# Kernel tuning notes

Measured on AMD Instinct MI355X. Metric: run time of the kernel, lower is better.

The kernel has to match this reference:

```python
import jax, jax.numpy as jnp
import numpy as np

EPS = 1e-6


def setup_inputs() -> dict:
    key = jax.random.key(0)
    ks = jax.random.split(key, 7)
    T, B, D, N = 512, 32, 1024, 128
    scale_w = (6.0 / (N + D)) ** 0.5  # xavier_uniform bound
    def w(k):
        return jax.random.uniform(k, (N, D), jnp.float32, -scale_w, scale_w)
    return {
        "x": jax.random.normal(ks[0], (T, B, D), jnp.float32),
        "S0": jnp.zeros((B, N, N), jnp.float32),
        "W_k": w(ks[1]),
        "W_v": w(ks[2]),
        "W_q": w(ks[3]),
        "W_erase": w(ks[4]),
        "W_write": w(ks[5]),
    }


def _ntm_forward(x, S0, W_k, W_v, W_q, W_erase, W_write):
    # Projections for all timesteps at once: (T, B, n_state)
    k = jnp.einsum('tbd,nd->tbn', x, W_k)
    v = jnp.einsum('tbd,nd->tbn', x, W_v)
    q = jnp.einsum('tbd,nd->tbn', x, W_q)
    erase = jnp.einsum('tbd,nd->tbn', x, W_erase)  # use_sigmoid=False: raw
    write = jnp.einsum('tbd,nd->tbn', x, W_write)

    def step(S, inp):
        k_t, v_t, q_t, e_t, w_t = inp
        k_norm = k_t / (jnp.linalg.norm(k_t, axis=-1, keepdims=True) + EPS)
        # S: (B, n, n); outer products via broadcasting
        erase_outer = e_t[:, :, None] * k_norm[:, None, :]
        write_outer = (w_t * v_t)[:, :, None] * k_norm[:, None, :]
        S_new = jnp.tanh(S * (1.0 - erase_outer) + write_outer)
        Sq = jnp.einsum('bij,bj->bi', S_new, q_t)
        out = Sq * jax.nn.silu(Sq)
        return S_new, out

    S_final, outputs = jax.lax.scan(step, S0, (k, v, q, erase, write))
    return outputs, S_final


def reference(x, S0, W_k, W_v, W_q, W_erase, W_write):
    return _ntm_forward(x, S0, W_k, W_v, W_q, W_erase, W_write)
```

## Files before the change

### kernel.cpp

```cpp
#include <hip/hip_runtime.h>
#include <hip/hip_bf16.h>


typedef __attribute__((ext_vector_type(8))) short bf16x8;
typedef __attribute__((ext_vector_type(4))) float f32x4;
typedef __attribute__((ext_vector_type(2))) float f32x2;
typedef __attribute__((ext_vector_type(4))) unsigned short u16x4;

static constexpr int T_STEPS = 512;
static constexpr int BATCH   = 32;
static constexpr int DDIM    = 1024;
static constexpr int NDIM    = 128;
static constexpr int LDC     = 5 * NDIM;
static constexpr int MROWS   = T_STEPS * BATCH;
static constexpr int OUT_N   = T_STEPS * BATCH * NDIM;

__device__ __forceinline__ void split2(float v, unsigned short& hi, unsigned short& lo) {
    unsigned u  = __builtin_bit_cast(unsigned, v);
    unsigned uh = u & 0xFFFF0000u;
    hi = (unsigned short)(uh >> 16);
    float d = v - __builtin_bit_cast(float, uh);
    lo = (unsigned short)(__builtin_bit_cast(unsigned, d) >> 16);
}

static constexpr int LSTR = 40;
static constexpr int OAH = 0, OAL = 128 * LSTR, OBH = 2 * 128 * LSTR, OBL = 3 * 128 * LSTR;

__global__ __launch_bounds__(256, 3) void gemm_kernel(
    const float* __restrict__ x,
    const float* __restrict__ w0, const float* __restrict__ w1,
    const float* __restrict__ w2, const float* __restrict__ w3,
    const float* __restrict__ w4,
    float* __restrict__ C)
{
    __shared__ unsigned short lds[4 * 128 * LSTR];

    const float* Ws[5] = {w0, w1, w2, w3, w4};
    const int id  = blockIdx.x;
    const int xcd = id & 7;
    const int kq  = id >> 3;
    const int bn  = kq % 5;
    const int bm  = (kq / 5) * 8 + xcd;

    const int tid  = threadIdx.x;
    const int wave = tid >> 6, lane = tid & 63;
    const int quad = lane >> 4, l16 = lane & 15;
    const int wm = (wave >> 1) * 64, wn = (wave & 1) * 64;
    const int m0 = bm * 128;
    const float* wsrc = Ws[bn];

    f32x4 acc[4][4];
#pragma unroll
    for (int i = 0; i < 4; ++i)
#pragma unroll
        for (int j = 0; j < 4; ++j) acc[i][j] = (f32x4)(0.0f);

    const int srow = tid >> 3;
    const int sc4  = tid & 7;
    const int fa = (wm + l16) * LSTR + quad * 8;
    const int fb = (wn + l16) * LSTR + quad * 8;

    for (int kk = 0; kk < 32; ++kk) {
#pragma unroll
        for (int i = 0; i < 4; ++i) {
            const int row = srow + i * 32;
            f32x4 va = *(const f32x4*)(x + (size_t)(m0 + row) * DDIM + kk * 32 + sc4 * 4);
            f32x4 vb = *(const f32x4*)(wsrc + (size_t)row * DDIM + kk * 32 + sc4 * 4);
            u16x4 ha, la, hb, lb;
#pragma unroll
            for (int j = 0; j < 4; ++j) {
                unsigned short h, l;
                split2(va[j], h, l); ha[j] = h; la[j] = l;
                split2(vb[j], h, l); hb[j] = h; lb[j] = l;
            }
            const int o = row * LSTR + sc4 * 4;
            *(u16x4*)&lds[OAH + o] = ha;
            *(u16x4*)&lds[OAL + o] = la;
            *(u16x4*)&lds[OBH + o] = hb;
            *(u16x4*)&lds[OBL + o] = lb;
        }
        __syncthreads();

        bf16x8 ah[4], al[4], bh[4], bl[4];
#pragma unroll
        for (int i = 0; i < 4; ++i) {
            ah[i] = *(const bf16x8*)&lds[OAH + fa + i * 16 * LSTR];
            al[i] = *(const bf16x8*)&lds[OAL + fa + i * 16 * LSTR];
            bh[i] = *(const bf16x8*)&lds[OBH + fb + i * 16 * LSTR];
            bl[i] = *(const bf16x8*)&lds[OBL + fb + i * 16 * LSTR];
        }
#pragma unroll
        for (int mi = 0; mi < 4; ++mi)
#pragma unroll
            for (int ni = 0; ni < 4; ++ni) {
                acc[mi][ni] = __builtin_amdgcn_mfma_f32_16x16x32_bf16(
                    ah[mi], bh[ni], acc[mi][ni], 0, 0, 0);
                acc[mi][ni] = __builtin_amdgcn_mfma_f32_16x16x32_bf16(
                    ah[mi], bl[ni], acc[mi][ni], 0, 0, 0);
                acc[mi][ni] = __builtin_amdgcn_mfma_f32_16x16x32_bf16(
                    al[mi], bh[ni], acc[mi][ni], 0, 0, 0);
            }
        __syncthreads();
    }

#pragma unroll
    for (int mi = 0; mi < 4; ++mi)
#pragma unroll
        for (int ni = 0; ni < 4; ++ni) {
            const int row = m0 + wm + mi * 16 + quad * 4;
            const int col = bn * 128 + wn + ni * 16 + l16;
#pragma unroll
            for (int r = 0; r < 4; ++r)
                C[(size_t)(row + r) * LDC + col] = acc[mi][ni][r];
        }
}

__global__ __launch_bounds__(256) void knorm_kernel(float* __restrict__ C)
{
    const int r    = blockIdx.x * 4 + (threadIdx.x >> 6);
    const int lane = threadIdx.x & 63;
    float* base = C + (size_t)r * LDC;

    f32x2 k2 = *(const f32x2*)(base + lane * 2);
    f32x2 v2 = *(const f32x2*)(base + NDIM + lane * 2);
    f32x2 w2 = *(const f32x2*)(base + 4 * NDIM + lane * 2);

    float ss = k2.x * k2.x + k2.y * k2.y;
#pragma unroll
    for (int off = 32; off >= 1; off >>= 1) ss += __shfl_xor(ss, off, 64);
    float inv = __builtin_amdgcn_rcpf(sqrtf(ss) + 1e-6f);

    f32x2 kn = {k2.x * inv, k2.y * inv};
    f32x2 wv = {v2.x * w2.x, v2.y * w2.y};
    *(f32x2*)(base + lane * 2) = kn;
    *(f32x2*)(base + NDIM + lane * 2) = wv;
}

__device__ __forceinline__ float tanh_fast(float xx) {
    float ex = __builtin_amdgcn_exp2f(xx * 2.8853900817779268f);
    float r  = __builtin_amdgcn_rcpf(ex + 1.0f);
    return fmaf(-2.0f, r, 1.0f);
}

template <int CTRL, int RMASK>
__device__ __forceinline__ float dpp_add(float x) {
    int yi = __builtin_amdgcn_update_dpp(
        0, __builtin_bit_cast(int, x), CTRL, RMASK, 0xF, true);
    return x + __builtin_bit_cast(float, yi);
}

__device__ __forceinline__ float dpp_reduce32(float x) {
    x = dpp_add<0xB1,  0xF>(x);
    x = dpp_add<0x4E,  0xF>(x);
    x = dpp_add<0x141, 0xF>(x);
    x = dpp_add<0x140, 0xF>(x);
    x = dpp_add<0x142, 0xA>(x);
    return x;
}

__global__ __launch_bounds__(256) void ntm_scan_kernel(
    const float* __restrict__ C, const float* __restrict__ S0,
    float* __restrict__ out)
{
    const int L    = blockIdx.x;
    const int b    = (L & 7) + 8 * ((L >> 3) & 3);
    const int row  = (L >> 5) * 8 + (threadIdx.x >> 5);
    const int g    = threadIdx.x & 31;
    const int col0 = g * 4;

    f32x4 S = *(const f32x4*)(S0 + ((size_t)b * NDIM + row) * NDIM + col0);

    const size_t STRIDE = (size_t)BATCH * LDC;
    const float* pb = C + (size_t)b * LDC;

    f32x4 kS[4], qS[4];
    float eS[4], wvS[4];

#pragma unroll
    for (int s = 0; s < 2; ++s) {
        const float* p = pb + (size_t)s * STRIDE;
        kS[s]  = *(const f32x4*)(p + col0);
        qS[s]  = *(const f32x4*)(p + 2 * NDIM + col0);
        eS[s]  = p[3 * NDIM + row];
        wvS[s] = p[NDIM + row];
    }

    float* op = out + (size_t)b * NDIM + row;

    for (int ti = 0; ti < T_STEPS / 4; ++ti) {
#pragma unroll
        for (int j = 0; j < 4; ++j) {
            const int t = ti * 4 + j;
            {
                int tp = t + 2;
                if (tp > T_STEPS - 1) tp = T_STEPS - 1;
                const float* p = pb + (size_t)tp * STRIDE;
                const int ps = (j + 2) & 3;
                kS[ps]  = *(const f32x4*)(p + col0);
                qS[ps]  = *(const f32x4*)(p + 2 * NDIM + col0);
                eS[ps]  = p[3 * NDIM + row];
                wvS[ps] = p[NDIM + row];
            }
            float dot = 0.0f;
#pragma unroll
            for (int u = 0; u < 4; ++u) {
                float t0  = fmaf(-eS[j], S[u], wvS[j]);
                float pre = fmaf(kS[j][u], t0, S[u]);
                S[u] = tanh_fast(pre);
                dot = fmaf(S[u], qS[j][u], dot);
            }
            dot = dpp_reduce32(dot);

            if ((threadIdx.x & 31) == 31)
                op[(size_t)t * BATCH * NDIM] = dot;
        }
    }

    *(f32x4*)(out + (size_t)T_STEPS * BATCH * NDIM
              + ((size_t)b * NDIM + row) * NDIM + col0) = S;
}

__global__ __launch_bounds__(256) void silu_kernel(float* __restrict__ out)
{
    const int i = blockIdx.x * 256 + threadIdx.x;
    f32x4 d = ((const f32x4*)out)[i];
    f32x4 y;
#pragma unroll
    for (int j = 0; j < 4; ++j) {
        float sg = __builtin_amdgcn_rcpf(
            1.0f + __builtin_amdgcn_exp2f(-d[j] * 1.4426950408889634f));
        y[j] = d[j] * d[j] * sg;
    }
    ((f32x4*)out)[i] = y;
}

extern "C" void kernel_launch(void* const* d_in, const int* in_sizes, int n_in,
                              void* d_out, int out_size, void* d_ws, size_t ws_size,
                              hipStream_t stream) {
    const float* x  = (const float*)d_in[0];
    const float* S0 = (const float*)d_in[1];
    const float* wk = (const float*)d_in[2];
    const float* wv = (const float*)d_in[3];
    const float* wq = (const float*)d_in[4];
    const float* we = (const float*)d_in[5];
    const float* ww = (const float*)d_in[6];
    float* out = (float*)d_out;
    float* C   = (float*)d_ws;

    gemm_kernel<<<640, 256, 0, stream>>>(x, wk, wv, wq, we, ww, C);
    knorm_kernel<<<MROWS / 4, 256, 0, stream>>>(C);
    ntm_scan_kernel<<<512, 256, 0, stream>>>(C, S0, out);
    silu_kernel<<<OUT_N / 1024, 256, 0, stream>>>(out);
}
```

Before: 307.9 us.

## Prefetch next K-tile into registers and stage split-bf16 MFMA passes in GEMM

The projection GEMM now loads the next K-slice of x and the weights from global memory into registers right after the LDS barrier, so those loads overlap with the current slice's MFMAs. The three split-precision MFMA passes (hi*hi, hi*lo, lo*hi) are reordered into separate loops, and the lo fragments are loaded from LDS only when needed. This is meant to hide global load latency and lower peak register pressure. In exchange it keeps extra prefetch registers live, which may affect occupancy at launch bounds of 3 waves per SIMD. The GEMM is only one of four kernels, and the serial scan likely dominates.

```diff
diff --git a/kernel.cpp b/kernel.cpp
--- a/kernel.cpp
+++ b/kernel.cpp
@@ -60,20 +60,29 @@
     const int fa = (wm + l16) * LSTR + quad * 8;
     const int fb = (wn + l16) * LSTR + quad * 8;
 
+    const float* xp[4];
+    const float* wp[4];
+#pragma unroll
+    for (int i = 0; i < 4; ++i) {
+        xp[i] = x    + (size_t)(m0 + srow + i * 32) * DDIM + sc4 * 4;
+        wp[i] = wsrc + (size_t)(srow + i * 32) * DDIM + sc4 * 4;
+    }
+
+    f32x4 ra[4], rb[4];
+#pragma unroll
+    for (int i = 0; i < 4; ++i) { ra[i] = *(const f32x4*)xp[i]; rb[i] = *(const f32x4*)wp[i]; }
+
     for (int kk = 0; kk < 32; ++kk) {
 #pragma unroll
         for (int i = 0; i < 4; ++i) {
-            const int row = srow + i * 32;
-            f32x4 va = *(const f32x4*)(x + (size_t)(m0 + row) * DDIM + kk * 32 + sc4 * 4);
-            f32x4 vb = *(const f32x4*)(wsrc + (size_t)row * DDIM + kk * 32 + sc4 * 4);
             u16x4 ha, la, hb, lb;
 #pragma unroll
             for (int j = 0; j < 4; ++j) {
                 unsigned short h, l;
-                split2(va[j], h, l); ha[j] = h; la[j] = l;
-                split2(vb[j], h, l); hb[j] = h; lb[j] = l;
+                split2(ra[i][j], h, l); ha[j] = h; la[j] = l;
+                split2(rb[i][j], h, l); hb[j] = h; lb[j] = l;
             }
-            const int o = row * LSTR + sc4 * 4;
+            const int o = (srow + i * 32) * LSTR + sc4 * 4;
             *(u16x4*)&lds[OAH + o] = ha;
             *(u16x4*)&lds[OAL + o] = la;
             *(u16x4*)&lds[OBH + o] = hb;
@@ -81,25 +90,49 @@
         }
         __syncthreads();
 
-        bf16x8 ah[4], al[4], bh[4], bl[4];
+        const int kn = (kk + 1 < 32) ? kk + 1 : 31;
+#pragma unroll
+        for (int i = 0; i < 4; ++i) {
+            ra[i] = *(const f32x4*)(xp[i] + kn * 32);
+            rb[i] = *(const f32x4*)(wp[i] + kn * 32);
+        }
+
+        bf16x8 ah[4], bh[4];
 #pragma unroll
         for (int i = 0; i < 4; ++i) {
             ah[i] = *(const bf16x8*)&lds[OAH + fa + i * 16 * LSTR];
-            al[i] = *(const bf16x8*)&lds[OAL + fa + i * 16 * LSTR];
             bh[i] = *(const bf16x8*)&lds[OBH + fb + i * 16 * LSTR];
-            bl[i] = *(const bf16x8*)&lds[OBL + fb + i * 16 * LSTR];
         }
 #pragma unroll
         for (int mi = 0; mi < 4; ++mi)
 #pragma unroll
-            for (int ni = 0; ni < 4; ++ni) {
+            for (int ni = 0; ni < 4; ++ni)
                 acc[mi][ni] = __builtin_amdgcn_mfma_f32_16x16x32_bf16(
                     ah[mi], bh[ni], acc[mi][ni], 0, 0, 0);
-                acc[mi][ni] = __builtin_amdgcn_mfma_f32_16x16x32_bf16(
-                    ah[mi], bl[ni], acc[mi][ni], 0, 0, 0);
-                acc[mi][ni] = __builtin_amdgcn_mfma_f32_16x16x32_bf16(
-                    al[mi], bh[ni], acc[mi][ni], 0, 0, 0);
-            }
+        {
+            bf16x8 bl[4];
+#pragma unroll
+            for (int i = 0; i < 4; ++i)
+                bl[i] = *(const bf16x8*)&lds[OBL + fb + i * 16 * LSTR];
+#pragma unroll
+            for (int mi = 0; mi < 4; ++mi)
+#pragma unroll
+                for (int ni = 0; ni < 4; ++ni)
+                    acc[mi][ni] = __builtin_amdgcn_mfma_f32_16x16x32_bf16(
+                        ah[mi], bl[ni], acc[mi][ni], 0, 0, 0);
+        }
+        {
+            bf16x8 al[4];
+#pragma unroll
+            for (int i = 0; i < 4; ++i)
+                al[i] = *(const bf16x8*)&lds[OAL + fa + i * 16 * LSTR];
+#pragma unroll
+            for (int mi = 0; mi < 4; ++mi)
+#pragma unroll
+                for (int ni = 0; ni < 4; ++ni)
+                    acc[mi][ni] = __builtin_amdgcn_mfma_f32_16x16x32_bf16(
+                        al[mi], bh[ni], acc[mi][ni], 0, 0, 0);
+        }
         __syncthreads();
     }
 
```

New measurement: 297.3 us. -3.4%, faster.
